# Kernel optimization log

Measured on AMD Instinct MI355X. Metric: run time of the kernel, lower is better.

Reference implementation:

```python
import jax, jax.numpy as jnp
import numpy as np

B, E, H, W, P, C = 2, 256, 192, 192, 16, 80
GRIDS = (40, 36, 24, 16, 12)
L = len(GRIDS)
MASK_W, CLS_W, ALPHA, GAMMA, EPS = 3.0, 1.0, 0.25, 2.0, 1e-4


def setup_inputs() -> dict:
    key = jax.random.key(0)
    ks = jax.random.split(key, 32)
    inp = {"mask_out": jax.random.normal(ks[0], (B, E, H, W), jnp.float32)}
    for i, g in enumerate(GRIDS):
        inp[f"kernel_l{i}"] = jax.random.normal(ks[1 + i], (B, g, g, E), jnp.float32) * 0.05
        inp[f"cate_l{i}"] = jax.random.uniform(ks[6 + i], (B, g, g, C), jnp.float32)
        inp[f"pos_l{i}"] = jax.random.randint(ks[11 + i], (B, P), 0, g * g, dtype=jnp.int32)
        inp[f"cate_t_l{i}"] = jax.random.randint(ks[16 + i], (B, g, g), -1, C, dtype=jnp.int32)
    # binary instance masks, image-major layout [B, L, P, H, W]
    inp["mask_targets"] = (jax.random.uniform(ks[21], (B, L, P, H, W)) > 0.9).astype(jnp.float32)
    return inp


def _forward(mask_out, kernels, cates, mask_targets, pos_idxs, cate_ts):
    # --- dynamic 1x1 conv: gather positive kernels and apply as batched matmul ---
    preds = []
    for kl, pl in zip(kernels, pos_idxs):
        g2 = kl.shape[1] * kl.shape[2]
        kflat = kl.reshape(B, g2, E)
        kp = jnp.take_along_axis(kflat, pl[:, :, None], axis=1)  # [B, P, E]
        preds.append(jnp.einsum('bpe,behw->bphw', kp, mask_out))  # F.conv2d 1x1
    preds = jnp.stack(preds)  # [L, B, P, H, W]  (level-major, matches torch cat order)

    # --- dice loss ---
    mp = jax.nn.sigmoid(preds).reshape(L * B * P, H * W)
    # NOTE: original code concatenates targets image-major (img, level) while preds
    # are level-major (level, img); we reproduce that pairing faithfully.
    mt = mask_targets.reshape(B * L * P, H * W)
    a = jnp.sum(mp * mt, axis=1)
    b = jnp.sum(mp * mp, axis=1)
    c = jnp.sum(mt * mt, axis=1)
    mask_loss = jnp.sum(1.0 - 2.0 * a / (b + c + 1e-4)) / (L * B * P)

    # --- focal loss on positive grid cells ---
    tgt = jnp.concatenate([t.reshape(-1) for t in cate_ts])            # [N]
    prd = jnp.concatenate([cl.reshape(-1, C) for cl in cates])          # [N, C]
    posm = (tgt > -1).astype(jnp.float32)
    p = jnp.clip(prd, EPS, 1.0 - EPS)
    gt = jax.nn.one_hot(jnp.clip(tgt, 0, C - 1), C, dtype=jnp.float32)
    af = jnp.where(gt == 1.0, ALPHA, 1.0 - ALPHA)
    pt = jnp.where(gt == 1.0, p, 1.0 - p)
    fw = af * (1.0 - pt) ** GAMMA
    ce = -(gt * jnp.log(p) + (1.0 - gt) * jnp.log(1.0 - p))
    cls_loss = jnp.sum(fw * ce * posm[:, None]) / jnp.sum(posm)

    return jnp.stack([MASK_W * mask_loss, CLS_W * cls_loss])  # [mask_loss, cls_loss]


def reference(mask_out, kernel_l0, kernel_l1, kernel_l2, kernel_l3, kernel_l4,
              cate_l0, cate_l1, cate_l2, cate_l3, cate_l4, mask_targets,
              pos_l0, pos_l1, pos_l2, pos_l3, pos_l4,
              cate_t_l0, cate_t_l1, cate_t_l2, cate_t_l3, cate_t_l4):
    return _forward(mask_out,
                    (kernel_l0, kernel_l1, kernel_l2, kernel_l3, kernel_l4),
                    (cate_l0, cate_l1, cate_l2, cate_l3, cate_l4),
                    mask_targets,
                    (pos_l0, pos_l1, pos_l2, pos_l3, pos_l4),
                    (cate_t_l0, cate_t_l1, cate_t_l2, cate_t_l3, cate_t_l4))
```

## Files before the change

### kernel.cpp

```cpp
#include <hip/hip_runtime.h>
#include <hip/hip_bf16.h>

namespace {

constexpr int kHW = 36864;
constexpr int kFocalElems = 7744 * 80;

typedef __attribute__((ext_vector_type(8))) short bf16x8;
typedef __attribute__((ext_vector_type(4))) float f32x4;

__device__ __forceinline__ unsigned short f2bf(float x) {
  return __builtin_bit_cast(unsigned short, __float2bfloat16(x));
}

__device__ __forceinline__ float wave_sum(float v) {
#pragma unroll
  for (int off = 32; off; off >>= 1) v += __shfl_xor(v, off, 64);
  return v;
}

__global__ __launch_bounds__(256, 2) void solov2_main(
    const float* __restrict__ mask_out,
    const float* __restrict__ k0, const float* __restrict__ k1,
    const float* __restrict__ k2, const float* __restrict__ k3,
    const float* __restrict__ k4,
    const int* __restrict__ q0, const int* __restrict__ q1,
    const int* __restrict__ q2, const int* __restrict__ q3,
    const int* __restrict__ q4,
    const float* __restrict__ mask_targets,
    float* __restrict__ acc) {
  const int b = blockIdx.y;
  const int pixbase = blockIdx.x * 128;
  const int lane = threadIdx.x & 63;
  const int wv = threadIdx.x >> 6;

  const float* kb[5] = {k0, k1, k2, k3, k4};
  const int* pb[5] = {q0, q1, q2, q3, q4};
  const int bg2[5] = {b * 1600, b * 1296, b * 576, b * 256, b * 144};

  __shared__ unsigned short klds[80][264];
  __shared__ float bred[4][240];

#pragma unroll 4
  for (int j0 = 0; j0 < 80; j0 += 2) {
    const int row = j0 + (threadIdx.x >> 7);
    const int ch = (threadIdx.x & 127) * 2;
    const int l = row >> 4, p = row & 15;
    const int pos = pb[l][b * 16 + p];
    const float2 kv =
        *(const float2*)(kb[l] + (size_t)(bg2[l] + pos) * 256 + ch);
    *(unsigned int*)&klds[row][ch] =
        (unsigned int)f2bf(kv.x) | ((unsigned int)f2bf(kv.y) << 16);
  }
  __syncthreads();

  const int hi8 = (lane >> 4) * 8;
  const int pxl = pixbase + wv * 32 + (lane & 15);
  const float* __restrict__ mop =
      mask_out + (size_t)b * 256 * kHW + (size_t)hi8 * kHW + pxl;

  f32x4 acc5[5][2];
#pragma unroll
  for (int mt = 0; mt < 5; ++mt)
#pragma unroll
    for (int nt = 0; nt < 2; ++nt) acc5[mt][nt] = (f32x4){0.f, 0.f, 0.f, 0.f};

#pragma unroll 2
  for (int ks = 0; ks < 8; ++ks) {
    float fb0[8], fb1[8];
#pragma unroll
    for (int j = 0; j < 8; ++j) {
      const size_t off = (size_t)(ks * 32 + j) * kHW;
      fb0[j] = mop[off];
      fb1[j] = mop[off + 16];
    }
    bf16x8 b0, b1;
#pragma unroll
    for (int j = 0; j < 8; ++j) {
      b0[j] = (short)f2bf(fb0[j]);
      b1[j] = (short)f2bf(fb1[j]);
    }
#pragma unroll
    for (int mt = 0; mt < 5; ++mt) {
      const bf16x8 a =
          *(const bf16x8*)&klds[mt * 16 + (lane & 15)][ks * 32 + hi8];
      acc5[mt][0] =
          __builtin_amdgcn_mfma_f32_16x16x32_bf16(a, b0, acc5[mt][0], 0, 0, 0);
      acc5[mt][1] =
          __builtin_amdgcn_mfma_f32_16x16x32_bf16(a, b1, acc5[mt][1], 0, 0, 0);
    }
  }

  const float* __restrict__ mtb = mask_targets;
#pragma unroll
  for (int mt = 0; mt < 5; ++mt) {
#pragma unroll
    for (int j = 0; j < 4; ++j) {
      const int row80 = mt * 16 + (lane >> 4) * 4 + j;
      const int r = (row80 >> 4) * 32 + b * 16 + (row80 & 15);
      const float x0 = acc5[mt][0][j];
      const float x1 = acc5[mt][1][j];
      const float mp0 = 1.f / (1.f + __expf(-x0));
      const float mp1 = 1.f / (1.f + __expf(-x1));
      const size_t base = (size_t)r * kHW + pxl;
      const float t0v = mtb[base];
      const float t1v = mtb[base + 16];
      float av = fmaf(mp0, t0v, mp1 * t1v);
      float bv = fmaf(mp0, mp0, mp1 * mp1);
      float cv = t0v + t1v;
#pragma unroll
      for (int m = 1; m <= 8; m <<= 1) {
        av += __shfl_xor(av, m, 64);
        bv += __shfl_xor(bv, m, 64);
        cv += __shfl_xor(cv, m, 64);
      }
      if ((lane & 15) == 0) {
        bred[wv][row80] = av;
        bred[wv][80 + row80] = bv;
        bred[wv][160 + row80] = cv;
      }
    }
  }
  __syncthreads();
  if (threadIdx.x < 240) {
    const int q = threadIdx.x / 80;
    const int row80 = threadIdx.x - q * 80;
    const int r = (row80 >> 4) * 32 + b * 16 + (row80 & 15);
    const float s = bred[0][threadIdx.x] + bred[1][threadIdx.x] +
                    bred[2][threadIdx.x] + bred[3][threadIdx.x];
    unsafeAtomicAdd(&acc[q * 160 + r], s);
  }
}

__global__ __launch_bounds__(256) void focal_kernel(
    const float* __restrict__ c0, const float* __restrict__ c1,
    const float* __restrict__ c2, const float* __restrict__ c3,
    const float* __restrict__ c4,
    const int* __restrict__ t0, const int* __restrict__ t1,
    const int* __restrict__ t2, const int* __restrict__ t3,
    const int* __restrict__ t4,
    float* __restrict__ acc) {
  float term = 0.f, np = 0.f;
  for (int idx = blockIdx.x * 256 + threadIdx.x; idx < kFocalElems;
       idx += gridDim.x * 256) {
    const int n = idx / 80;
    const int c = idx - n * 80;
    int t;
    const float* crow;
    if (n < 3200) {
      t = t0[n]; crow = c0 + (size_t)n * 80;
    } else if (n < 5792) {
      const int o = n - 3200; t = t1[o]; crow = c1 + (size_t)o * 80;
    } else if (n < 6944) {
      const int o = n - 5792; t = t2[o]; crow = c2 + (size_t)o * 80;
    } else if (n < 7456) {
      const int o = n - 6944; t = t3[o]; crow = c3 + (size_t)o * 80;
    } else {
      const int o = n - 7456; t = t4[o]; crow = c4 + (size_t)o * 80;
    }
    if (t > -1) {
      float pv = crow[c];
      pv = fminf(fmaxf(pv, 1e-4f), 1.f - 1e-4f);
      const bool gm = (c == t);
      const float af = gm ? 0.25f : 0.75f;
      const float pt = gm ? pv : 1.f - pv;
      const float om = 1.f - pt;
      term = fmaf(af * om * om, -__logf(pt), term);
      if (c == 0) np += 1.f;
    }
  }
  term = wave_sum(term);
  np = wave_sum(np);
  __shared__ float st[8];
  const int wid = threadIdx.x >> 6;
  if ((threadIdx.x & 63) == 0) {
    st[wid] = term;
    st[4 + wid] = np;
  }
  __syncthreads();
  if (threadIdx.x == 0) {
    unsafeAtomicAdd(&acc[480], st[0] + st[1] + st[2] + st[3]);
    unsafeAtomicAdd(&acc[481], st[4] + st[5] + st[6] + st[7]);
  }
}

__global__ void zero_kernel(float* __restrict__ acc) {
  const int i = blockIdx.x * 256 + threadIdx.x;
  if (i < 482) acc[i] = 0.f;
}

__global__ __launch_bounds__(64) void finalize_kernel(
    const float* __restrict__ acc, float* __restrict__ out) {
  const int tid = threadIdx.x;
  float s = 0.f;
#pragma unroll
  for (int rr = 0; rr < 3; ++rr) {
    const int r = tid + rr * 64;
    if (r < 160) {
      const float a = acc[r];
      const float bb = acc[160 + r];
      const float cc = acc[320 + r];
      s += 1.f - 2.f * a / (bb + cc + 1e-4f);
    }
  }
  s = wave_sum(s);
  if (tid == 0) {
    out[0] = 3.0f * (s / 160.f);
    out[1] = acc[480] / acc[481];
  }
}

}

extern "C" void kernel_launch(void* const* d_in, const int* in_sizes, int n_in,
                              void* d_out, int out_size, void* d_ws,
                              size_t ws_size, hipStream_t stream) {
  const float* mask_out = (const float*)d_in[0];
  const float* k[5];
  const float* cc[5];
  const int* pp[5];
  const int* tt[5];
  for (int i = 0; i < 5; ++i) {
    k[i] = (const float*)d_in[1 + 4 * i];
    cc[i] = (const float*)d_in[2 + 4 * i];
    pp[i] = (const int*)d_in[3 + 4 * i];
    tt[i] = (const int*)d_in[4 + 4 * i];
  }
  const float* mt = (const float*)d_in[21];
  float* acc = (float*)d_ws;
  float* out = (float*)d_out;

  hipLaunchKernelGGL(zero_kernel, dim3(2), dim3(256), 0, stream, acc);
  hipLaunchKernelGGL(solov2_main, dim3(288, 2), dim3(256), 0, stream,
                     mask_out, k[0], k[1], k[2], k[3], k[4], pp[0], pp[1],
                     pp[2], pp[3], pp[4], mt, acc);
  hipLaunchKernelGGL(focal_kernel, dim3(320), dim3(256), 0, stream, cc[0],
                     cc[1], cc[2], cc[3], cc[4], tt[0], tt[1], tt[2], tt[3],
                     tt[4], acc);
  hipLaunchKernelGGL(finalize_kernel, dim3(1), dim3(64), 0, stream, acc, out);
}
```

Measured before the change: 67.16 us.

## Hoist kernel gather into separate kernel and software-pipeline mask_out loads

Moves the per-block gather and bf16 conversion of the 80 positive kernels into a small standalone kernel that writes a bf16 weight buffer to workspace. The main kernel now reads its A operands directly from global memory (cached), not LDS. It halves pixels per block to 64, doubling the grid and raising the occupancy hint to 4. It also triple-buffers the mask_out loads across K steps to overlap global latency with MFMA. This trades an extra launch and per-block redundant global reads of weights for removing repeated gather/sync work and LDS use.

```diff
diff --git a/kernel.cpp b/kernel.cpp
--- a/kernel.cpp
+++ b/kernel.cpp
@@ -19,102 +19,102 @@
   return v;
 }
 
-__global__ __launch_bounds__(256, 2) void solov2_main(
-    const float* __restrict__ mask_out,
+__global__ __launch_bounds__(128) void gather_k(
     const float* __restrict__ k0, const float* __restrict__ k1,
     const float* __restrict__ k2, const float* __restrict__ k3,
     const float* __restrict__ k4,
     const int* __restrict__ q0, const int* __restrict__ q1,
     const int* __restrict__ q2, const int* __restrict__ q3,
     const int* __restrict__ q4,
+    unsigned short* __restrict__ kbf) {
+  const int b = blockIdx.y;
+  const int row = blockIdx.x;
+  const int l = row >> 4, p = row & 15;
+  const float* kb[5] = {k0, k1, k2, k3, k4};
+  const int* pb[5] = {q0, q1, q2, q3, q4};
+  const int bg2[5] = {b * 1600, b * 1296, b * 576, b * 256, b * 144};
+  const int pos = pb[l][b * 16 + p];
+  const int ch = threadIdx.x * 2;
+  const float2 kv = *(const float2*)(kb[l] + (size_t)(bg2[l] + pos) * 256 + ch);
+  *(unsigned int*)&kbf[((size_t)b * 80 + row) * 256 + ch] =
+      (unsigned int)f2bf(kv.x) | ((unsigned int)f2bf(kv.y) << 16);
+}
+
+__global__ __launch_bounds__(256, 4) void solov2_main(
+    const float* __restrict__ mask_out,
+    const unsigned short* __restrict__ kbf,
     const float* __restrict__ mask_targets,
     float* __restrict__ acc) {
   const int b = blockIdx.y;
-  const int pixbase = blockIdx.x * 128;
   const int lane = threadIdx.x & 63;
   const int wv = threadIdx.x >> 6;
-
-  const float* kb[5] = {k0, k1, k2, k3, k4};
-  const int* pb[5] = {q0, q1, q2, q3, q4};
-  const int bg2[5] = {b * 1600, b * 1296, b * 576, b * 256, b * 144};
-
-  __shared__ unsigned short klds[80][264];
-  __shared__ float bred[4][240];
-
-#pragma unroll 4
-  for (int j0 = 0; j0 < 80; j0 += 2) {
-    const int row = j0 + (threadIdx.x >> 7);
-    const int ch = (threadIdx.x & 127) * 2;
-    const int l = row >> 4, p = row & 15;
-    const int pos = pb[l][b * 16 + p];
-    const float2 kv =
-        *(const float2*)(kb[l] + (size_t)(bg2[l] + pos) * 256 + ch);
-    *(unsigned int*)&klds[row][ch] =
-        (unsigned int)f2bf(kv.x) | ((unsigned int)f2bf(kv.y) << 16);
-  }
-  __syncthreads();
-
+  const int px16 = lane & 15;
   const int hi8 = (lane >> 4) * 8;
-  const int pxl = pixbase + wv * 32 + (lane & 15);
+  const int pxl = blockIdx.x * 64 + wv * 16 + px16;
+
   const float* __restrict__ mop =
       mask_out + (size_t)b * 256 * kHW + (size_t)hi8 * kHW + pxl;
-
-  f32x4 acc5[5][2];
-#pragma unroll
-  for (int mt = 0; mt < 5; ++mt)
-#pragma unroll
-    for (int nt = 0; nt < 2; ++nt) acc5[mt][nt] = (f32x4){0.f, 0.f, 0.f, 0.f};
-
-#pragma unroll 2
-  for (int ks = 0; ks < 8; ++ks) {
-    float fb0[8], fb1[8];
-#pragma unroll
-    for (int j = 0; j < 8; ++j) {
-      const size_t off = (size_t)(ks * 32 + j) * kHW;
-      fb0[j] = mop[off];
-      fb1[j] = mop[off + 16];
-    }
-    bf16x8 b0, b1;
-#pragma unroll
-    for (int j = 0; j < 8; ++j) {
-      b0[j] = (short)f2bf(fb0[j]);
-      b1[j] = (short)f2bf(fb1[j]);
-    }
-#pragma unroll
-    for (int mt = 0; mt < 5; ++mt) {
-      const bf16x8 a =
-          *(const bf16x8*)&klds[mt * 16 + (lane & 15)][ks * 32 + hi8];
-      acc5[mt][0] =
-          __builtin_amdgcn_mfma_f32_16x16x32_bf16(a, b0, acc5[mt][0], 0, 0, 0);
-      acc5[mt][1] =
-          __builtin_amdgcn_mfma_f32_16x16x32_bf16(a, b1, acc5[mt][1], 0, 0, 0);
-    }
-  }
-
-  const float* __restrict__ mtb = mask_targets;
+  const unsigned short* __restrict__ ka =
+      kbf + ((size_t)b * 80 + px16) * 256 + hi8;
+
+  __shared__ float bred[4][240];
+
+  f32x4 a5[5];
+#pragma unroll
+  for (int mt = 0; mt < 5; ++mt) a5[mt] = (f32x4){0.f, 0.f, 0.f, 0.f};
+
+  float pf0[8], pf1[8], pf2[8];
+
+#define PF(BUF, KS)                                                         \
+  {                                                                         \
+    _Pragma("unroll") for (int j = 0; j < 8; ++j)                           \
+        BUF[j] = mop[(size_t)((KS) * 32 + j) * kHW];                        \
+  }
+
+#define STEP(BUF, KS)                                                       \
+  {                                                                         \
+    bf16x8 bb;                                                              \
+    _Pragma("unroll") for (int j = 0; j < 8; ++j)                           \
+        bb[j] = (short)f2bf(BUF[j]);                                        \
+    _Pragma("unroll") for (int mt = 0; mt < 5; ++mt) {                      \
+      const bf16x8 af = *(const bf16x8*)(ka + mt * 4096 + (KS) * 32);       \
+      a5[mt] = __builtin_amdgcn_mfma_f32_16x16x32_bf16(af, bb, a5[mt],      \
+                                                       0, 0, 0);            \
+    }                                                                       \
+  }
+
+  PF(pf0, 0);
+  PF(pf1, 1);
+  PF(pf2, 2); STEP(pf0, 0);
+  PF(pf0, 3); STEP(pf1, 1);
+  PF(pf1, 4); STEP(pf2, 2);
+  PF(pf2, 5); STEP(pf0, 3);
+  PF(pf0, 6); STEP(pf1, 4);
+  PF(pf1, 7); STEP(pf2, 5);
+  STEP(pf0, 6);
+  STEP(pf1, 7);
+#undef PF
+#undef STEP
+
 #pragma unroll
   for (int mt = 0; mt < 5; ++mt) {
 #pragma unroll
     for (int j = 0; j < 4; ++j) {
       const int row80 = mt * 16 + (lane >> 4) * 4 + j;
       const int r = (row80 >> 4) * 32 + b * 16 + (row80 & 15);
-      const float x0 = acc5[mt][0][j];
-      const float x1 = acc5[mt][1][j];
-      const float mp0 = 1.f / (1.f + __expf(-x0));
-      const float mp1 = 1.f / (1.f + __expf(-x1));
-      const size_t base = (size_t)r * kHW + pxl;
-      const float t0v = mtb[base];
-      const float t1v = mtb[base + 16];
-      float av = fmaf(mp0, t0v, mp1 * t1v);
-      float bv = fmaf(mp0, mp0, mp1 * mp1);
-      float cv = t0v + t1v;
+      const float x0 = a5[mt][j];
+      const float mp = 1.f / (1.f + __expf(-x0));
+      const float tv = mask_targets[(size_t)r * kHW + pxl];
+      float av = mp * tv;
+      float bv = mp * mp;
+      float cv = tv;
 #pragma unroll
       for (int m = 1; m <= 8; m <<= 1) {
         av += __shfl_xor(av, m, 64);
         bv += __shfl_xor(bv, m, 64);
         cv += __shfl_xor(cv, m, 64);
       }
-      if ((lane & 15) == 0) {
+      if (px16 == 0) {
         bred[wv][row80] = av;
         bred[wv][80 + row80] = bv;
         bred[wv][160 + row80] = cv;
@@ -228,12 +228,15 @@
   }
   const float* mt = (const float*)d_in[21];
   float* acc = (float*)d_ws;
+  unsigned short* kbf = (unsigned short*)((float*)d_ws + 512);
   float* out = (float*)d_out;
 
   hipLaunchKernelGGL(zero_kernel, dim3(2), dim3(256), 0, stream, acc);
-  hipLaunchKernelGGL(solov2_main, dim3(288, 2), dim3(256), 0, stream,
-                     mask_out, k[0], k[1], k[2], k[3], k[4], pp[0], pp[1],
-                     pp[2], pp[3], pp[4], mt, acc);
+  hipLaunchKernelGGL(gather_k, dim3(80, 2), dim3(128), 0, stream,
+                     k[0], k[1], k[2], k[3], k[4], pp[0], pp[1], pp[2], pp[3],
+                     pp[4], kbf);
+  hipLaunchKernelGGL(solov2_main, dim3(576, 2), dim3(256), 0, stream,
+                     mask_out, kbf, mt, acc);
   hipLaunchKernelGGL(focal_kernel, dim3(320), dim3(256), 0, stream, cc[0],
                      cc[1], cc[2], cc[3], cc[4], tt[0], tt[1], tt[2], tt[3],
                      tt[4], acc);
```

After: 73.93 us. 1.1x slower.
